# Optimization experiments

Measured on AMD Instinct MI355X. Metric: run time of the kernel, lower is better.

The kernel has to match this reference:

```python
import jax, jax.numpy as jnp
import numpy as np

N_HEAD = 16
EPS = 1e-5
ROPE_BASE = 10000.0


def setup_inputs() -> dict:
    key = jax.random.key(0)
    ks = jax.random.split(key, 6)
    B, T, C = 2, 2048, 1024
    s = 0.02  # typical GPT init scale
    return {
        "x": jax.random.normal(ks[0], (B, T, C), dtype=jnp.float32),
        "wq": jax.random.normal(ks[1], (C, C), dtype=jnp.float32) * s,
        "wk": jax.random.normal(ks[2], (C, C), dtype=jnp.float32) * s,
        "wv": jax.random.normal(ks[3], (C, C), dtype=jnp.float32) * s,
        "wproj": jax.random.normal(ks[4], (C, C), dtype=jnp.float32) * s,
        "g_rms": jnp.ones((C // N_HEAD,), dtype=jnp.float32),
    }


def reference(x, wq, wk, wv, wproj, g_rms):
    B, T, C = x.shape
    H = N_HEAD
    hd = C // H

    # QKV projections (torch Linear: y = x @ W.T), split into heads -> [B,T,H,hd]
    q = (x @ wq.T).reshape(B, T, H, hd)
    k = (x @ wk.T).reshape(B, T, H, hd)
    v = (x @ wv.T).reshape(B, T, H, hd)

    # RMSNorm over head_dim on q and k
    def rms(t):
        var = jnp.mean(t * t, axis=-1, keepdims=True) + EPS
        return g_rms * (t * jax.lax.rsqrt(var))

    q, k = rms(q), rms(k)

    # Rotary embeddings: cos/sin cached in bf16 in the original -> bf16 round-trip
    inv_freq = 1.0 / (ROPE_BASE ** (jnp.arange(0, hd, 2, dtype=jnp.float32) / hd))
    freqs = jnp.outer(jnp.arange(T, dtype=jnp.float32), inv_freq)  # [T, hd/2]
    cos = jnp.cos(freqs).astype(jnp.bfloat16).astype(jnp.float32)[None, :, None, :]
    sin = jnp.sin(freqs).astype(jnp.bfloat16).astype(jnp.float32)[None, :, None, :]

    def rope(u):
        d = hd // 2
        u1, u2 = u[..., :d], u[..., d:]
        return jnp.concatenate([u1 * cos + u2 * sin, -u1 * sin + u2 * cos], axis=-1)

    q, k = rope(q), rope(k)

    # Attention: float ones attn_mask => constant +1.0 bias (softmax-invariant);
    # NOT causal (is_causal defaults False); dropout_p = 0.
    qh = q.transpose(0, 2, 1, 3)  # [B,H,T,hd]
    kh = k.transpose(0, 2, 1, 3)
    vh = v.transpose(0, 2, 1, 3)
    scale = 1.0 / jnp.sqrt(jnp.float32(hd))
    scores = jnp.einsum('bhtd,bhsd->bhts', qh, kh) * scale + 1.0  # [B,H,T,T]
    attn = jax.nn.softmax(scores, axis=-1)
    y = jnp.einsum('bhts,bhsd->bhtd', attn, vh)

    y = y.transpose(0, 2, 1, 3).reshape(B, T, C)
    return y @ wproj.T
```

## Files before the change

kernel.cpp:

```cpp
#include <hip/hip_runtime.h>
#include <hip/hip_bf16.h>
#include <stdint.h>

typedef __attribute__((ext_vector_type(8))) short short8;
typedef __attribute__((ext_vector_type(4))) float f32x4;
typedef __attribute__((ext_vector_type(16))) float f32x16;
typedef __attribute__((ext_vector_type(4))) unsigned short ushort4v;
typedef __attribute__((ext_vector_type(4))) unsigned int uint4v;

#define TT 2048
#define HH 16
#define CCdim 1024
#define BT 4096
#define LOG2E 1.44269504088896f

__device__ inline unsigned short f2bf(float f) {
  unsigned u = __float_as_uint(f);
  u += 0x7FFF + ((u >> 16) & 1);
  return (unsigned short)(u >> 16);
}
__device__ inline float bf2f(unsigned short s) {
  return __uint_as_float(((unsigned)s) << 16);
}
__device__ inline unsigned pack2(float a, float b) {
  return (unsigned)f2bf(a) | ((unsigned)f2bf(b) << 16);
}
__device__ inline unsigned cvtpk(float lo, float hi) {
  unsigned r;
  asm("v_cvt_pk_bf16_f32 %0, %1, %2" : "=v"(r) : "v"(lo), "v"(hi));
  return r;
}
__device__ inline void plswap(unsigned &a, unsigned &b) {
  asm("v_permlane32_swap_b32 %0, %1" : "+v"(a), "+v"(b));
}

__device__ inline void gload16(const unsigned short* g, unsigned short* l) {
  __builtin_amdgcn_global_load_lds((const __attribute__((address_space(1))) void*)g,
                                   (__attribute__((address_space(3))) void*)l, 16, 0, 0);
}

#define VMB(N) do { asm volatile("s_waitcnt vmcnt(" #N ")" ::: "memory"); \
                    __builtin_amdgcn_s_barrier(); \
                    __builtin_amdgcn_sched_barrier(0); } while (0)

__global__ __launch_bounds__(256) void prep(const float* __restrict__ x, const float* __restrict__ wq,
                     const float* __restrict__ wk, const float* __restrict__ wv,
                     const float* __restrict__ wp, unsigned short* __restrict__ xb,
                     unsigned short* __restrict__ wqkv, unsigned short* __restrict__ wpb,
                     float2* __restrict__ tab) {
  long idx = ((long)blockIdx.x * 256 + threadIdx.x) * 4;
  const long NX = (long)BT * CCdim;
  const long NW = (long)CCdim * CCdim;
  auto cvt4 = [](const float* src, unsigned short* dst, long off) {
    float4 v = *(const float4*)(src + off);
    ushort4v o = { f2bf(v.x), f2bf(v.y), f2bf(v.z), f2bf(v.w) };
    *(ushort4v*)(dst + off) = o;
  };
  if (idx < NX) { cvt4(x, xb, idx); return; }
  idx -= NX;
  if (idx < NW) { cvt4(wq, wqkv, idx); return; }
  idx -= NW;
  if (idx < NW) { cvt4(wk, wqkv + NW, idx); return; }
  idx -= NW;
  if (idx < NW) { cvt4(wv, wqkv + 2 * NW, idx); return; }
  idx -= NW;
  if (idx < NW) { cvt4(wp, wpb, idx); return; }
  idx -= NW;
  if (idx < (long)TT * 32) {
#pragma unroll
    for (int j = 0; j < 4; ++j) {
      long e = idx + j;
      int t = (int)(e >> 5), i = (int)(e & 31);
      float invf = powf(10000.0f, -(float)i / 32.0f);
      float a = (float)t * invf;
      tab[e] = make_float2(bf2f(f2bf(cosf(a))), bf2f(f2bf(sinf(a))));
    }
  }
}

__global__ __launch_bounds__(512) void gemm_qkv(const unsigned short* __restrict__ A,
                                                const unsigned short* __restrict__ W,
                                                const float* __restrict__ g,
                                                const float2* __restrict__ tab,
                                                unsigned short* __restrict__ Qh,
                                                unsigned short* __restrict__ Kp,
                                                unsigned short* __restrict__ Vp) {
  __shared__ __align__(16) char smem[49152];
  unsigned short* const S0 = (unsigned short*)smem;
  unsigned short* const S1 = S0 + 8192;
  unsigned short* const S2 = S0 + 16384;
  typedef unsigned short (*Earr)[32][68];
  Earr E = (Earr)smem;
  const int K = 1024;
  const int tid = threadIdx.x;
  const int lane = tid & 63;
  const int wid = tid >> 6;
  const int wr = wid >> 1, wc = wid & 1;
  const int bid0 = blockIdx.y * 24 + blockIdx.x;
  const int xcd = bid0 & 7, ii = bid0 >> 3;
  const int bx = (xcd & 1) * 12 + ii % 12;
  const int by = (xcd >> 1) * 8 + ii / 12;
  const int m0 = by * 128;
  const int n0 = bx * 128;

  f32x4 acc[2][4] = {};

  const int srow0 = tid >> 2;
  const int cgrp = tid & 3;
  const int cd = (cgrp ^ ((srow0 >> 1) & 3)) * 8;
  const unsigned short* Arow = A + (long)(m0 + srow0) * K + cd;
  const unsigned short* Wrow = W + (long)(n0 + srow0) * K + cd;

  auto stage = [&](unsigned short* Ab, int kt) {
    const int kof = kt * 32;
    gload16(Arow + kof, Ab + wid * 512);
    gload16(Wrow + kof, Ab + 4096 + wid * 512);
  };
  auto compute = [&](const unsigned short* Ab) {
    const unsigned short* Wb = Ab + 4096;
    short8 af[2], bf[4];
#pragma unroll
    for (int mi = 0; mi < 2; ++mi) {
      int r = wr * 32 + mi * 16 + (lane & 15);
      af[mi] = *(const short8*)&Ab[r * 32 + (((lane >> 4) ^ ((r >> 1) & 3)) * 8)];
    }
#pragma unroll
    for (int nj = 0; nj < 4; ++nj) {
      int r = wc * 64 + nj * 16 + (lane & 15);
      bf[nj] = *(const short8*)&Wb[r * 32 + (((lane >> 4) ^ ((r >> 1) & 3)) * 8)];
    }
#pragma unroll
    for (int mi = 0; mi < 2; ++mi)
#pragma unroll
      for (int nj = 0; nj < 4; ++nj)
        acc[mi][nj] = __builtin_amdgcn_mfma_f32_16x16x32_bf16(af[mi], bf[nj], acc[mi][nj], 0, 0, 0);
  };

  stage(S0, 0);
  stage(S1, 1);
  for (int tb = 0; tb < 30; tb += 3) {
    VMB(2); stage(S2, tb + 2); compute(S0);
    VMB(2); stage(S0, tb + 3); compute(S1);
    VMB(2); stage(S1, tb + 4); compute(S2);
  }
  VMB(2); compute(S0);
  VMB(0); compute(S1);
  __syncthreads();

  const int type = bx >> 3;
  const int c0 = n0 + wc * 64;
  const int b = m0 >> 11;
  const int t0w = (m0 & 2047) + wr * 32;
  const int bh = b * 16 + ((c0 >> 6) & 15);
  const int cl = lane & 15;
  const int hi4 = lane >> 4;

  if (type < 2) {
    float gv0 = g[cl], gv1 = g[cl + 16], gv2 = g[cl + 32], gv3 = g[cl + 48];
    const float qs = (type == 0) ? 0.125f * LOG2E : 1.0f;
#pragma unroll
    for (int mi = 0; mi < 2; ++mi)
#pragma unroll
      for (int j = 0; j < 4; ++j) {
        float x0 = acc[mi][0][j], x1 = acc[mi][1][j], x2 = acc[mi][2][j], x3 = acc[mi][3][j];
        float ss = x0 * x0 + x1 * x1 + x2 * x2 + x3 * x3;
        ss += __shfl_xor(ss, 1); ss += __shfl_xor(ss, 2);
        ss += __shfl_xor(ss, 4); ss += __shfl_xor(ss, 8);
        float ri = rsqrtf(ss * (1.0f / 64.0f) + 1e-5f);
        float xn0 = x0 * ri * gv0, xn1 = x1 * ri * gv1;
        float xn2 = x2 * ri * gv2, xn3 = x3 * ri * gv3;
        int t = t0w + mi * 16 + 4 * hi4 + j;
        float2 cs0 = tab[t * 32 + cl];
        float2 cs1 = tab[t * 32 + cl + 16];
        int lr = mi * 16 + 4 * hi4 + j;
        E[wid][lr][cl]      = f2bf((xn0 * cs0.x + xn2 * cs0.y) * qs);
        E[wid][lr][cl + 16] = f2bf((xn1 * cs1.x + xn3 * cs1.y) * qs);
        E[wid][lr][cl + 32] = f2bf((xn2 * cs0.x - xn0 * cs0.y) * qs);
        E[wid][lr][cl + 48] = f2bf((xn3 * cs1.x - xn1 * cs1.y) * qs);
      }
  } else {
#pragma unroll
    for (int mi = 0; mi < 2; ++mi)
#pragma unroll
      for (int j = 0; j < 4; ++j) {
        int lr = mi * 16 + 4 * hi4 + j;
        E[wid][lr][cl]      = f2bf(acc[mi][0][j]);
        E[wid][lr][cl + 16] = f2bf(acc[mi][1][j]);
        E[wid][lr][cl + 32] = f2bf(acc[mi][2][j]);
        E[wid][lr][cl + 48] = f2bf(acc[mi][3][j]);
      }
  }
  __syncthreads();

  if (type == 0) {
    for (int row = 0; row < 32; ++row) {
      int t = t0w + row;
      Qh[((long)bh * TT + t) * 64 + lane] = E[wid][row][lane];
    }
  } else if (type == 1) {
    for (int row = 0; row < 32; ++row) {
      int t = t0w + row;
      Kp[(((long)bh * 64 + (t >> 5)) * 4 + (lane >> 4)) * 512
         + ((t & 31) + 32 * ((lane >> 3) & 1)) * 8 + (lane & 7)] = E[wid][row][lane];
    }
  } else {
    unsigned short* base = Vp + ((long)bh * 64 + (t0w >> 5)) * 2048;
#pragma unroll
    for (int it = 0; it < 4; ++it) {
      int id = it * 64 + lane;
      int cc = it & 1, sd = (it >> 1) & 1;
      int d = sd * 32 + (lane & 31);
      int tl = cc * 16 + (lane >> 5) * 8;
      short8 o;
#pragma unroll
      for (int jj = 0; jj < 8; ++jj) o[jj] = (short)E[wid][tl + jj][d];
      *(short8*)(base + (long)id * 8) = o;
    }
  }
}

__global__ __launch_bounds__(512) void gemm_bt(const unsigned short* __restrict__ A,
                                               const unsigned short* __restrict__ W,
                                               float* __restrict__ C, int ldc) {
  __shared__ __align__(16) unsigned short Sbuf[3][8192];
  unsigned short* const S0 = &Sbuf[0][0];
  unsigned short* const S1 = &Sbuf[1][0];
  unsigned short* const S2 = &Sbuf[2][0];
  const int K = 1024;
  const int tid = threadIdx.x;
  const int lane = tid & 63;
  const int wid = tid >> 6;
  const int wr = wid >> 1, wc = wid & 1;
  const int bid0 = blockIdx.y * 8 + blockIdx.x;
  const int xcd = bid0 & 7, ii = bid0 >> 3;
  const int m0 = (xcd * 4 + ii / 8) * 128;
  const int n0 = (ii & 7) * 128;

  f32x4 acc[2][4] = {};

  const int srow0 = tid >> 2;
  const int cgrp = tid & 3;
  const int cd = (cgrp ^ ((srow0 >> 1) & 3)) * 8;
  const unsigned short* Arow = A + (long)(m0 + srow0) * K + cd;
  const unsigned short* Wrow = W + (long)(n0 + srow0) * K + cd;

  auto stage = [&](unsigned short* Ab, int kt) {
    const int kof = kt * 32;
    gload16(Arow + kof, Ab + wid * 512);
    gload16(Wrow + kof, Ab + 4096 + wid * 512);
  };
  auto compute = [&](const unsigned short* Ab) {
    const unsigned short* Wb = Ab + 4096;
    short8 af[2], bf[4];
#pragma unroll
    for (int mi = 0; mi < 2; ++mi) {
      int r = wr * 32 + mi * 16 + (lane & 15);
      af[mi] = *(const short8*)&Ab[r * 32 + (((lane >> 4) ^ ((r >> 1) & 3)) * 8)];
    }
#pragma unroll
    for (int nj = 0; nj < 4; ++nj) {
      int r = wc * 64 + nj * 16 + (lane & 15);
      bf[nj] = *(const short8*)&Wb[r * 32 + (((lane >> 4) ^ ((r >> 1) & 3)) * 8)];
    }
#pragma unroll
    for (int mi = 0; mi < 2; ++mi)
#pragma unroll
      for (int nj = 0; nj < 4; ++nj)
        acc[mi][nj] = __builtin_amdgcn_mfma_f32_16x16x32_bf16(af[mi], bf[nj], acc[mi][nj], 0, 0, 0);
  };

  stage(S0, 0);
  stage(S1, 1);
  for (int tb = 0; tb < 30; tb += 3) {
    VMB(2); stage(S2, tb + 2); compute(S0);
    VMB(2); stage(S0, tb + 3); compute(S1);
    VMB(2); stage(S1, tb + 4); compute(S2);
  }
  VMB(2); compute(S0);
  VMB(0); compute(S1);

#pragma unroll
  for (int mi = 0; mi < 2; ++mi)
#pragma unroll
    for (int nj = 0; nj < 4; ++nj)
#pragma unroll
      for (int j = 0; j < 4; ++j) {
        int rr = m0 + wr * 32 + mi * 16 + 4 * (lane >> 4) + j;
        int ncol = n0 + wc * 64 + nj * 16 + (lane & 15);
        C[(long)rr * ldc + ncol] = acc[mi][nj][j];
      }
}

__global__ __launch_bounds__(256, 2) void attn(const unsigned short* __restrict__ Qh,
                                               const unsigned short* __restrict__ Kp,
                                               const unsigned short* __restrict__ Vp,
                                               unsigned short* __restrict__ Y) {
  __shared__ __align__(16) float Obuf[2][64][65];
  __shared__ float Ebuf[2][64];
  const int lane = threadIdx.x & 63;
  const int wid = threadIdx.x >> 6;
  const int l = blockIdx.x;
  const int xcd = l & 7, j = l >> 3;
  const int bh_ = xcd + (j >> 4) * 8;
  const int w = (bh_ * 16 + (j & 15)) * 4 + wid;
  const int half = w & 1;
  const int qt = (w >> 1) & 31;
  const int bh = w >> 6;
  const long bhT = (long)bh * TT;
  const int q0 = qt * 64;
  const int l31 = lane & 31;
  const int hk = (lane >> 5) * 8;

  short8 qf[4], qg[4];
  {
    const unsigned short* qp = Qh + (bhT + q0 + l31) * 64 + hk;
#pragma unroll
    for (int c = 0; c < 4; ++c) {
      qf[c] = *(const short8*)(qp + c * 16);
      qg[c] = *(const short8*)(qp + 2048 + c * 16);
    }
  }

  const unsigned short* kp = Kp + ((long)(bh * 64 + half * 32)) * 2048 + lane * 8;
  const unsigned short* vp = Vp + ((long)(bh * 64 + half * 32)) * 2048 + lane * 8;

  f32x16 oacc0 = {}, oacc1 = {}, oacc2 = {}, oacc3 = {};
  float ell = 0.f, ell2 = 0.f;

  short8 kA[4], vA0[2], vA1[2], kB[4], vB0[2], vB1[2];
#pragma unroll
  for (int c = 0; c < 4; ++c) kA[c] = *(const short8*)(kp + c * 512);
#pragma unroll
  for (int c = 0; c < 2; ++c) {
    vA0[c] = *(const short8*)(vp + c * 512);
    vA1[c] = *(const short8*)(vp + 1024 + c * 512);
  }

  auto body = [&](short8 (&kc)[4], short8 (&v0c)[2], short8 (&v1c)[2],
                  short8 (&knx)[4], short8 (&v0n)[2], short8 (&v1n)[2], int tn) {
    const unsigned short* kpn = kp + tn * 2048;
    const unsigned short* vpn = vp + tn * 2048;
#pragma unroll
    for (int c = 0; c < 4; ++c) knx[c] = *(const short8*)(kpn + c * 512);
#pragma unroll
    for (int c = 0; c < 2; ++c) {
      v0n[c] = *(const short8*)(vpn + c * 512);
      v1n[c] = *(const short8*)(vpn + 1024 + c * 512);
    }

    __builtin_amdgcn_s_setprio(1);
    f32x16 s = {}, s2 = {};
#pragma unroll
    for (int c = 0; c < 4; ++c) {
      s  = __builtin_amdgcn_mfma_f32_32x32x16_bf16(kc[c], qf[c], s, 0, 0, 0);
      s2 = __builtin_amdgcn_mfma_f32_32x32x16_bf16(kc[c], qg[c], s2, 0, 0, 0);
    }
    __builtin_amdgcn_s_setprio(0);

#pragma unroll
    for (int r = 0; r < 16; ++r) s[r] = __builtin_amdgcn_exp2f(s[r]);
#pragma unroll
    for (int r = 0; r < 16; ++r) s2[r] = __builtin_amdgcn_exp2f(s2[r]);
    {
      float t0 = s[0] + s[1], t1 = s[2] + s[3], t2s = s[4] + s[5], t3 = s[6] + s[7];
      float t4 = s[8] + s[9], t5 = s[10] + s[11], t6 = s[12] + s[13], t7 = s[14] + s[15];
      t0 += t1; t2s += t3; t4 += t5; t6 += t7;
      ell += (t0 + t2s) + (t4 + t6);
    }
    {
      float t0 = s2[0] + s2[1], t1 = s2[2] + s2[3], t2s = s2[4] + s2[5], t3 = s2[6] + s2[7];
      float t4 = s2[8] + s2[9], t5 = s2[10] + s2[11], t6 = s2[12] + s2[13], t7 = s2[14] + s2[15];
      t0 += t1; t2s += t3; t4 += t5; t6 += t7;
      ell2 += (t0 + t2s) + (t4 + t6);
    }

    unsigned a0 = cvtpk(s[0], s[1]),   a1 = cvtpk(s[2], s[3]);
    unsigned a2 = cvtpk(s[4], s[5]),   a3 = cvtpk(s[6], s[7]);
    unsigned a4 = cvtpk(s[8], s[9]),   a5 = cvtpk(s[10], s[11]);
    unsigned a6 = cvtpk(s[12], s[13]), a7 = cvtpk(s[14], s[15]);
    plswap(a0, a2); plswap(a1, a3); plswap(a4, a6); plswap(a5, a7);
    uint4v f0 = { a0, a1, a2, a3 };
    uint4v f1 = { a4, a5, a6, a7 };
    short8 pf0 = __builtin_bit_cast(short8, f0);
    short8 pf1 = __builtin_bit_cast(short8, f1);

    unsigned b0 = cvtpk(s2[0], s2[1]),   b1 = cvtpk(s2[2], s2[3]);
    unsigned b2 = cvtpk(s2[4], s2[5]),   b3 = cvtpk(s2[6], s2[7]);
    unsigned b4 = cvtpk(s2[8], s2[9]),   b5 = cvtpk(s2[10], s2[11]);
    unsigned b6 = cvtpk(s2[12], s2[13]), b7 = cvtpk(s2[14], s2[15]);
    plswap(b0, b2); plswap(b1, b3); plswap(b4, b6); plswap(b5, b7);
    uint4v g0 = { b0, b1, b2, b3 };
    uint4v g1 = { b4, b5, b6, b7 };
    short8 pg0 = __builtin_bit_cast(short8, g0);
    short8 pg1 = __builtin_bit_cast(short8, g1);

    __builtin_amdgcn_s_setprio(1);
    oacc0 = __builtin_amdgcn_mfma_f32_32x32x16_bf16(v0c[0], pf0, oacc0, 0, 0, 0);
    oacc0 = __builtin_amdgcn_mfma_f32_32x32x16_bf16(v0c[1], pf1, oacc0, 0, 0, 0);
    oacc1 = __builtin_amdgcn_mfma_f32_32x32x16_bf16(v1c[0], pf0, oacc1, 0, 0, 0);
    oacc1 = __builtin_amdgcn_mfma_f32_32x32x16_bf16(v1c[1], pf1, oacc1, 0, 0, 0);
    oacc2 = __builtin_amdgcn_mfma_f32_32x32x16_bf16(v0c[0], pg0, oacc2, 0, 0, 0);
    oacc2 = __builtin_amdgcn_mfma_f32_32x32x16_bf16(v0c[1], pg1, oacc2, 0, 0, 0);
    oacc3 = __builtin_amdgcn_mfma_f32_32x32x16_bf16(v1c[0], pg0, oacc3, 0, 0, 0);
    oacc3 = __builtin_amdgcn_mfma_f32_32x32x16_bf16(v1c[1], pg1, oacc3, 0, 0, 0);
    __builtin_amdgcn_s_setprio(0);
  };

  for (int t = 0; t < 32; t += 2) {
    int t1 = t + 1;
    int t2 = (t < 30) ? (t + 2) : 31;
    body(kA, vA0, vA1, kB, vB0, vB1, t1);
    body(kB, vB0, vB1, kA, vA0, vA1, t2);
  }

  float ellf  = ell + __shfl_xor(ell, 32);
  float ellf2 = ell2 + __shfl_xor(ell2, 32);
  const int pl = wid >> 1;
  const int dhalf = 4 * (lane >> 5);

  if (half) {
#pragma unroll
    for (int i = 0; i < 8; ++i) {
      int d = (2 * i & 3) + 8 * (i >> 1) + dhalf;
      *(float2*)&Obuf[pl][l31][d]           = make_float2(oacc0[2 * i], oacc0[2 * i + 1]);
      *(float2*)&Obuf[pl][l31][32 + d]      = make_float2(oacc1[2 * i], oacc1[2 * i + 1]);
      *(float2*)&Obuf[pl][l31 + 32][d]      = make_float2(oacc2[2 * i], oacc2[2 * i + 1]);
      *(float2*)&Obuf[pl][l31 + 32][32 + d] = make_float2(oacc3[2 * i], oacc3[2 * i + 1]);
    }
    if (lane < 32) { Ebuf[pl][l31] = ellf; Ebuf[pl][l31 + 32] = ellf2; }
  }
  __syncthreads();
  if (!half) {
    const int b = bh >> 4, h = bh & 15;
    float r1 = 1.0f / (ellf + Ebuf[pl][l31]);
    float r2 = 1.0f / (ellf2 + Ebuf[pl][l31 + 32]);
    long base1 = ((long)b * TT + q0 + l31) * CCdim + h * 64;
    long base2 = base1 + (long)32 * CCdim;
#pragma unroll
    for (int i = 0; i < 8; ++i) {
      int d = (2 * i & 3) + 8 * (i >> 1) + dhalf;
      *(unsigned*)&Y[base1 + d] =
        pack2((oacc0[2 * i] + Obuf[pl][l31][d]) * r1,
              (oacc0[2 * i + 1] + Obuf[pl][l31][d + 1]) * r1);
      *(unsigned*)&Y[base1 + 32 + d] =
        pack2((oacc1[2 * i] + Obuf[pl][l31][32 + d]) * r1,
              (oacc1[2 * i + 1] + Obuf[pl][l31][32 + d + 1]) * r1);
      *(unsigned*)&Y[base2 + d] =
        pack2((oacc2[2 * i] + Obuf[pl][l31 + 32][d]) * r2,
              (oacc2[2 * i + 1] + Obuf[pl][l31 + 32][d + 1]) * r2);
      *(unsigned*)&Y[base2 + 32 + d] =
        pack2((oacc3[2 * i] + Obuf[pl][l31 + 32][32 + d]) * r2,
              (oacc3[2 * i + 1] + Obuf[pl][l31 + 32][32 + d + 1]) * r2);
    }
  }
}

extern "C" void kernel_launch(void* const* d_in, const int* in_sizes, int n_in,
                              void* d_out, int out_size, void* d_ws, size_t ws_size,
                              hipStream_t stream) {
  const float* x  = (const float*)d_in[0];
  const float* wq = (const float*)d_in[1];
  const float* wk = (const float*)d_in[2];
  const float* wv = (const float*)d_in[3];
  const float* wp = (const float*)d_in[4];
  const float* g  = (const float*)d_in[5];

  char* w = (char*)d_ws;
  unsigned short* xb   = (unsigned short*)w; w += (long)BT * CCdim * 2;
  unsigned short* wqkv = (unsigned short*)w; w += (long)3 * CCdim * CCdim * 2;
  unsigned short* wpb  = (unsigned short*)w; w += (long)CCdim * CCdim * 2;
  unsigned short* qh   = (unsigned short*)w; w += (long)BT * CCdim * 2;
  unsigned short* kp   = (unsigned short*)w; w += (long)BT * CCdim * 2;
  unsigned short* vp   = (unsigned short*)w; w += (long)BT * CCdim * 2;
  unsigned short* yb   = (unsigned short*)w; w += (long)BT * CCdim * 2;
  float2* tab          = (float2*)w;         w += (long)TT * 32 * 8;

  long total = ((long)BT * CCdim + 4L * CCdim * CCdim + (long)TT * 32) / 4;
  int pblocks = (int)((total + 255) / 256);
  prep<<<pblocks, 256, 0, stream>>>(x, wq, wk, wv, wp, xb, wqkv, wpb, tab);
  gemm_qkv<<<dim3(24, 32), 512, 0, stream>>>(xb, wqkv, g, tab, qh, kp, vp);
  attn<<<512, 256, 0, stream>>>(qh, kp, vp, yb);
  gemm_bt<<<dim3(8, 32), 512, 0, stream>>>(yb, wpb, (float*)d_out, 1024);
}
```

Baseline: 109.4 us.

## Software-pipeline attention loop: overlap next QK MFMA with current softmax/PV

Restructures the attention inner loop into stages: K loads, QK^T MFMAs, and the exp/PV finish step are split into separate lambdas and interleaved so that the QK product for tile t+1 is issued before the softmax and PV of tile t. This is meant to hide the exp and packing VALU latency behind independent MFMA work and to decouple K and V prefetch. It raises register pressure, since two score tiles are held at once, which may reduce occupancy or cause spills.

Measured after the change: 110.3 us. Within noise of the previous version (+0.8%).

```diff
diff --git a/kernel.cpp b/kernel.cpp
--- a/kernel.cpp
+++ b/kernel.cpp
@@ -327,36 +327,33 @@
   f32x16 oacc0 = {}, oacc1 = {}, oacc2 = {}, oacc3 = {};
   float ell = 0.f, ell2 = 0.f;
 
-  short8 kA[4], vA0[2], vA1[2], kB[4], vB0[2], vB1[2];
-#pragma unroll
-  for (int c = 0; c < 4; ++c) kA[c] = *(const short8*)(kp + c * 512);
-#pragma unroll
-  for (int c = 0; c < 2; ++c) {
-    vA0[c] = *(const short8*)(vp + c * 512);
-    vA1[c] = *(const short8*)(vp + 1024 + c * 512);
-  }
-
-  auto body = [&](short8 (&kc)[4], short8 (&v0c)[2], short8 (&v1c)[2],
-                  short8 (&knx)[4], short8 (&v0n)[2], short8 (&v1n)[2], int tn) {
-    const unsigned short* kpn = kp + tn * 2048;
-    const unsigned short* vpn = vp + tn * 2048;
-#pragma unroll
-    for (int c = 0; c < 4; ++c) knx[c] = *(const short8*)(kpn + c * 512);
+  short8 kA[4], kB[4], vA0[2], vA1[2], vB0[2], vB1[2];
+
+  auto loadK = [&](short8 (&kd)[4], int t) {
+    const unsigned short* kpn = kp + t * 2048;
+#pragma unroll
+    for (int c = 0; c < 4; ++c) kd[c] = *(const short8*)(kpn + c * 512);
+  };
+  auto loadV = [&](short8 (&v0)[2], short8 (&v1)[2], int t) {
+    const unsigned short* vpn = vp + t * 2048;
 #pragma unroll
     for (int c = 0; c < 2; ++c) {
-      v0n[c] = *(const short8*)(vpn + c * 512);
-      v1n[c] = *(const short8*)(vpn + 1024 + c * 512);
-    }
-
+      v0[c] = *(const short8*)(vpn + c * 512);
+      v1[c] = *(const short8*)(vpn + 1024 + c * 512);
+    }
+  };
+  auto qk2 = [&](short8 (&kc)[4], f32x16 &d1, f32x16 &d2) {
+    f32x16 a = {}, b = {};
     __builtin_amdgcn_s_setprio(1);
-    f32x16 s = {}, s2 = {};
 #pragma unroll
     for (int c = 0; c < 4; ++c) {
-      s  = __builtin_amdgcn_mfma_f32_32x32x16_bf16(kc[c], qf[c], s, 0, 0, 0);
-      s2 = __builtin_amdgcn_mfma_f32_32x32x16_bf16(kc[c], qg[c], s2, 0, 0, 0);
+      a = __builtin_amdgcn_mfma_f32_32x32x16_bf16(kc[c], qf[c], a, 0, 0, 0);
+      b = __builtin_amdgcn_mfma_f32_32x32x16_bf16(kc[c], qg[c], b, 0, 0, 0);
     }
     __builtin_amdgcn_s_setprio(0);
-
+    d1 = a; d2 = b;
+  };
+  auto finish = [&](f32x16 &s, f32x16 &s2, short8 (&v0c)[2], short8 (&v1c)[2]) {
 #pragma unroll
     for (int r = 0; r < 16; ++r) s[r] = __builtin_amdgcn_exp2f(s[r]);
 #pragma unroll
@@ -406,12 +403,27 @@
     __builtin_amdgcn_s_setprio(0);
   };
 
-  for (int t = 0; t < 32; t += 2) {
-    int t1 = t + 1;
-    int t2 = (t < 30) ? (t + 2) : 31;
-    body(kA, vA0, vA1, kB, vB0, vB1, t1);
-    body(kB, vB0, vB1, kA, vA0, vA1, t2);
-  }
+  loadK(kA, 0);
+  loadV(vA0, vA1, 0);
+  f32x16 s1, s2v, u1, u2;
+  qk2(kA, s1, s2v);
+  loadK(kB, 1);
+
+  for (int p = 0; p < 15; ++p) {
+    int t = 2 * p + 1;
+    loadK(kA, t + 1);
+    loadV(vB0, vB1, t);
+    qk2(kB, u1, u2);
+    finish(s1, s2v, vA0, vA1);
+    loadK(kB, t + 2);
+    loadV(vA0, vA1, t + 1);
+    qk2(kA, s1, s2v);
+    finish(u1, u2, vB0, vB1);
+  }
+  loadV(vB0, vB1, 31);
+  qk2(kB, u1, u2);
+  finish(s1, s2v, vA0, vA1);
+  finish(u1, u2, vB0, vB1);
 
   float ellf  = ell + __shfl_xor(ell, 32);
   float ellf2 = ell2 + __shfl_xor(ell2, 32);
```
